# Performance work log

Measured on AMD Instinct MI355X. Metric: run time of the kernel, lower is better.

## Reference

```python
import jax, jax.numpy as jnp
import numpy as np

CS = [32, 32, 64, 128, 256, 256, 128, 96, 96]
NC = 19
N0, N1, N2, N3, N4 = 50000, 20000, 8000, 3200, 1300


def build_shapes():
    cs = CS
    def rb(ci, co):
        t = [(27, ci, co), (27, co, co)]
        if ci != co:
            t.append((ci, co))  # 1x1 shortcut conv
        return t
    s = [(27, 4, cs[0]), (27, cs[0], cs[0])]                       # stem
    s += [(8, cs[0], cs[0])] + rb(cs[0], cs[1]) + rb(cs[1], cs[1])  # stage1
    s += [(8, cs[1], cs[1])] + rb(cs[1], cs[2]) + rb(cs[2], cs[2])  # stage2
    s += [(8, cs[2], cs[2])] + rb(cs[2], cs[3]) + rb(cs[3], cs[3])  # stage3
    s += [(8, cs[3], cs[3])] + rb(cs[3], cs[4]) + rb(cs[4], cs[4])  # stage4
    s += [(8, cs[4], cs[5])] + rb(cs[5] + cs[3], cs[5]) + rb(cs[5], cs[5])  # up1
    s += [(8, cs[5], cs[6])] + rb(cs[6] + cs[2], cs[6]) + rb(cs[6], cs[6])  # up2
    s += [(8, cs[6], cs[7])] + rb(cs[7] + cs[1], cs[7]) + rb(cs[7], cs[7])  # up3
    s += [(8, cs[7], cs[8])] + rb(cs[8] + cs[0], cs[8]) + rb(cs[8], cs[8])  # up4
    s += [(cs[8], NC), (NC,), (cs[8], cs[8]), (cs[8],), (cs[8], 128), (128,)]
    return s

P_TOTAL = sum(int(np.prod(sh)) for sh in build_shapes())


def _bn(x):
    # train-mode BatchNorm, gamma=1 beta=0 (set by weight_initialization)
    return (x - x.mean(0)) * jax.lax.rsqrt(jnp.var(x, 0) + 1e-5)


def _spconv(x, nbr, W):
    # sparse conv as gather-GEMM-scatter over K kernel offsets.
    # x: [Nin, Cin], nbr: [Nout, K] row indices into x, W: [K, Cin, Cout]
    acc0 = jnp.zeros((nbr.shape[0], W.shape[-1]), x.dtype)
    def step(acc, kw):
        idx, Wk = kw
        return acc + x[idx] @ Wk, None
    acc, _ = jax.lax.scan(step, acc0, (nbr.T, W))
    return acc


def _spdeconv(x, parent, off, W):
    # transposed ks=2 stride=2 conv: each fine voxel has exactly one coarse
    # parent and one kernel-offset id. out[i] = x[parent[i]] @ W[off[i]]
    y = jnp.einsum('nc,kcd->nkd', x[parent], W)  # [Nf, 8, Cout]
    return jnp.take_along_axis(y, off[:, None, None], axis=1)[:, 0, :]


def _cbr(x, nbr, W):
    return jax.nn.relu(_bn(_spconv(x, nbr, W)))


def _resblock(x, nbr, take, ci, co):
    w1 = take(); w2 = take()
    h = _bn(_spconv(jax.nn.relu(_bn(_spconv(x, nbr, w1))), nbr, w2))
    s = x if ci == co else _bn(x @ take())
    return jax.nn.relu(h + s)


def _forward(x, nbr0, nbr1, nbr2, nbr3, nbr4, d1, d2, d3, d4,
             u1p, u1o, u2p, u2o, u3p, u3o, u4p, u4o, params):
    parts = []
    o = 0
    for sh in build_shapes():
        n = int(np.prod(sh))
        parts.append(params[o:o + n].reshape(sh))
        o += n
    it = iter(parts)
    take = lambda: next(it)
    cs = CS
    x0 = _cbr(x, nbr0, take()); x0 = _cbr(x0, nbr0, take())            # stem
    h = _cbr(x0, d1, take())
    h = _resblock(h, nbr1, take, cs[0], cs[1]); x1 = _resblock(h, nbr1, take, cs[1], cs[1])
    h = _cbr(x1, d2, take())
    h = _resblock(h, nbr2, take, cs[1], cs[2]); x2 = _resblock(h, nbr2, take, cs[2], cs[2])
    h = _cbr(x2, d3, take())
    h = _resblock(h, nbr3, take, cs[2], cs[3]); x3 = _resblock(h, nbr3, take, cs[3], cs[3])
    h = _cbr(x3, d4, take())
    h = _resblock(h, nbr4, take, cs[3], cs[4]); x4 = _resblock(h, nbr4, take, cs[4], cs[4])
    y = jax.nn.relu(_bn(_spdeconv(x4, u1p, u1o, take())))
    y = jnp.concatenate([y, x3], 1)
    y = _resblock(y, nbr3, take, cs[5] + cs[3], cs[5]); y = _resblock(y, nbr3, take, cs[5], cs[5])
    y = jax.nn.relu(_bn(_spdeconv(y, u2p, u2o, take())))
    y = jnp.concatenate([y, x2], 1)
    y = _resblock(y, nbr2, take, cs[6] + cs[2], cs[6]); y = _resblock(y, nbr2, take, cs[6], cs[6])
    y = jax.nn.relu(_bn(_spdeconv(y, u3p, u3o, take())))
    y = jnp.concatenate([y, x1], 1)
    y = _resblock(y, nbr1, take, cs[7] + cs[1], cs[7]); y = _resblock(y, nbr1, take, cs[7], cs[7])
    y = jax.nn.relu(_bn(_spdeconv(y, u4p, u4o, take())))
    y = jnp.concatenate([y, x0], 1)
    y = _resblock(y, nbr0, take, cs[8] + cs[0], cs[8]); y = _resblock(y, nbr0, take, cs[8], cs[8])
    wc = take(); bc = take(); w1 = take(); b1 = take(); w2 = take(); b2 = take()
    out = y @ wc + bc                             # classifier logits [N0, NC]
    feat = jax.nn.relu(y @ w1 + b1) @ w2 + b2     # projection head [N0, 128]
    return out, feat


def setup_inputs() -> dict:
    key = jax.random.key(0)
    ks = jax.random.split(key, 20)
    ri = lambda k, shape, hi: jax.random.randint(k, shape, 0, hi, dtype=jnp.int32)
    return {
        'x': jax.random.normal(ks[0], (N0, 4), jnp.float32),
        'nbr0': ri(ks[1], (N0, 27), N0), 'nbr1': ri(ks[2], (N1, 27), N1),
        'nbr2': ri(ks[3], (N2, 27), N2), 'nbr3': ri(ks[4], (N3, 27), N3),
        'nbr4': ri(ks[5], (N4, 27), N4),
        'd1': ri(ks[6], (N1, 8), N0), 'd2': ri(ks[7], (N2, 8), N1),
        'd3': ri(ks[8], (N3, 8), N2), 'd4': ri(ks[9], (N4, 8), N3),
        'u1p': ri(ks[10], (N3,), N4), 'u1o': ri(ks[11], (N3,), 8),
        'u2p': ri(ks[12], (N2,), N3), 'u2o': ri(ks[13], (N2,), 8),
        'u3p': ri(ks[14], (N1,), N2), 'u3o': ri(ks[15], (N1,), 8),
        'u4p': ri(ks[16], (N0,), N1), 'u4o': ri(ks[17], (N0,), 8),
        'params': jax.random.normal(ks[18], (P_TOTAL,), jnp.float32) * 0.05,
    }


def reference(x, nbr0, nbr1, nbr2, nbr3, nbr4, d1, d2, d3, d4,
              u1p, u1o, u2p, u2o, u3p, u3o, u4p, u4o, params):
    return _forward(x, nbr0, nbr1, nbr2, nbr3, nbr4, d1, d2, d3, d4,
                    u1p, u1o, u2p, u2o, u3p, u3o, u4p, u4o, params)
```

## Files before the change

kernel.cpp:

```cpp
#include <hip/hip_runtime.h>
#include <hip/hip_bf16.h>
#include <stdint.h>

typedef __hip_bfloat16 hbf;
typedef unsigned short u16;
typedef __attribute__((ext_vector_type(8))) short bfrag;
typedef __attribute__((ext_vector_type(4))) float f4;

#define NP0 50000
#define NP1 20000
#define NP2 8000
#define NP3 3200
#define NP4 1300

static inline int cdiv(int a, int b) { return (a + b - 1) / b; }

static __device__ __forceinline__ float u2f(u16 u) { return __uint_as_float(((unsigned)u) << 16); }
static __device__ __forceinline__ u16 f2u(float f) {
  hbf h = __float2bfloat16(f);
  u16 r; __builtin_memcpy(&r, &h, 2); return r;
}
static __device__ __forceinline__ float pload(const void* P, int isbf, size_t i) {
  return isbf ? u2f(((const u16*)P)[i]) : ((const float*)P)[i];
}


struct PrepD {
  long cpre;
  long src;
  long dst;
  int K, CI, CO, CB32, NT16, pad;
};

__global__ void k_sniff(const void* __restrict__ xraw, int* __restrict__ flagp) {
  __shared__ float smax[256];
  const u16* u = (const u16*)xraw;
  float m = 0.f;
  for (int i = threadIdx.x; i < 2048; i += 256) {
    float v = u2f(u[2 * i]);
    if (isnan(v) || isinf(v)) m = 1e30f; else m = fmaxf(m, fabsf(v));
  }
  smax[threadIdx.x] = m;
  __syncthreads();
  for (int s = 128; s > 0; s >>= 1) {
    if (threadIdx.x < s) smax[threadIdx.x] = fmaxf(smax[threadIdx.x], smax[threadIdx.x + s]);
    __syncthreads();
  }
  if (threadIdx.x == 0) *flagp = (smax[0] < 1e4f) ? 1 : 0;
}

__global__ __launch_bounds__(256) void k_prep_all(
    const void* __restrict__ P, const int* __restrict__ flagp, u16* __restrict__ W,
    const PrepD* __restrict__ T, int NL, long totalC, long totalE)
{
  int f = *flagp;
  int L = 0;
  for (long c = (long)blockIdx.x * 256 + threadIdx.x; c < totalC; c += (long)gridDim.x * 256) {
    while (L + 1 < NL && c >= T[L + 1].cpre) ++L;
    PrepD d = T[L];
    long lc = c - d.cpre;
    int lane = (int)(lc & 63); long t = lc >> 6;
    int nt = (int)(t % d.NT16); t /= d.NT16;
    int cb = (int)(t % d.CB32); int k = (int)(t / d.CB32);
    int co = nt * 16 + (lane & 15);
    int cib = cb * 32 + (lane >> 4) * 8;
    u16 hi[8], lo[8];
#pragma unroll
    for (int j = 0; j < 8; ++j) {
      int ci = cib + j; float v = 0.f;
      if (ci < d.CI && co < d.CO) v = pload(P, f, d.src + ((size_t)k * d.CI + ci) * d.CO + co);
      u16 h = f2u(v);
      hi[j] = h;
      lo[j] = f2u(v - u2f(h));
    }
    *(bfrag*)(W + d.dst + lc * 8) = *(const bfrag*)hi;
    *(bfrag*)(W + totalE + d.dst + lc * 8) = *(const bfrag*)lo;
  }
}

__global__ __launch_bounds__(256) void k_prep_frag(
    const void* __restrict__ P, const int* __restrict__ flagp, u16* __restrict__ W,
    long src, long halfel, int K, int CI, int CO, int CB32, int NT16)
{
  int f = *flagp;
  long total = (long)K * CB32 * NT16 * 64;
  for (long c = (long)blockIdx.x * 256 + threadIdx.x; c < total; c += (long)gridDim.x * 256) {
    int lane = (int)(c & 63); long t = c >> 6;
    int nt = (int)(t % NT16); t /= NT16;
    int cb = (int)(t % CB32); int k = (int)(t / CB32);
    int co = nt * 16 + (lane & 15);
    int cib = cb * 32 + (lane >> 4) * 8;
    u16 hi[8], lo[8];
#pragma unroll
    for (int j = 0; j < 8; ++j) {
      int ci = cib + j; float v = 0.f;
      if (ci < CI && co < CO) v = pload(P, f, src + ((size_t)k * CI + ci) * CO + co);
      u16 h = f2u(v);
      hi[j] = h;
      lo[j] = f2u(v - u2f(h));
    }
    *(bfrag*)(W + c * 8) = *(const bfrag*)hi;
    *(bfrag*)(W + halfel + c * 8) = *(const bfrag*)lo;
  }
}

__global__ void k_prep_bias(const void* __restrict__ P, const int* __restrict__ flagp,
                            float* __restrict__ B, long src, int n)
{
  int f = *flagp;
  int i = blockIdx.x * 256 + threadIdx.x;
  if (i < n) B[i] = pload(P, f, src + i);
}

__global__ void k_pad(const void* __restrict__ xraw, const int* __restrict__ flagp,
                      float* __restrict__ Xp, int N)
{
  int f = *flagp; int total = N * 32;
  for (int i = blockIdx.x * 256 + threadIdx.x; i < total; i += gridDim.x * 256) {
    int n = i >> 5, cc = i & 31;
    Xp[i] = (cc < 4) ? pload(xraw, f, (size_t)n * 4 + cc) : 0.f;
  }
}

template<int NT>
__global__ __launch_bounds__(256) void k_conv_mfma(
    const float* __restrict__ X, const int* __restrict__ nbr,
    const u16* __restrict__ Wp, long halfel, float* __restrict__ Y,
    const float* __restrict__ bias, int relu, const int* __restrict__ flagp,
    int N, int K, int CB32, int NT16, int CO, int XS, int tlen, int atomic)
{
  const int f = *flagp;
  const int lane = threadIdx.x & 63;
  const int wv = threadIdx.x >> 6;
  const int rowbase = blockIdx.x * 128 + wv * 32;
  const int ntb = blockIdx.y * NT;
  const int ml = lane & 15;
  const int quad = lane >> 4;
  const int ktot = K * CB32;
  const int t0 = blockIdx.z * tlen;
  const int t1 = (t0 + tlen < ktot) ? (t0 + tlen) : ktot;

  f4 acc[2][NT];
#pragma unroll
  for (int i = 0; i < 2; ++i)
#pragma unroll
    for (int j = 0; j < NT; ++j) acc[i][j] = (f4)(0.f);

  int k = t0 / CB32;
  int cb = t0 - k * CB32;
  int idx[2];
  bool fresh = true;

  if (f) {
    for (int t = t0; t < t1; ++t) {
      if (fresh) {
#pragma unroll
        for (int mt = 0; mt < 2; ++mt) {
          int r = rowbase + mt * 16 + ml;
          idx[mt] = (r < N) ? (nbr ? nbr[(size_t)r * K + k] : r) : 0;
        }
        fresh = false;
      }
      const u16* WH = Wp + (size_t)t * NT16 * 512;
      bfrag bh[NT];
#pragma unroll
      for (int nt = 0; nt < NT; ++nt) {
        size_t o = ((size_t)(ntb + nt) * 64 + lane) * 8;
        bh[nt] = *(const bfrag*)(WH + o);
      }
      bfrag ahi[2], alo[2];
#pragma unroll
      for (int mt = 0; mt < 2; ++mt) {
        const float* ap = X + (size_t)idx[mt] * XS + cb * 32 + quad * 8;
        float4 q0 = *(const float4*)ap;
        float4 q1 = *(const float4*)(ap + 4);
        float av[8] = {q0.x, q0.y, q0.z, q0.w, q1.x, q1.y, q1.z, q1.w};
        u16 hi8[8], lo8[8];
#pragma unroll
        for (int j = 0; j < 8; ++j) {
          u16 hh = f2u(av[j]);
          hi8[j] = hh;
          lo8[j] = f2u(av[j] - u2f(hh));
        }
        __builtin_memcpy(&ahi[mt], hi8, 16);
        __builtin_memcpy(&alo[mt], lo8, 16);
      }
#pragma unroll
      for (int mt = 0; mt < 2; ++mt)
#pragma unroll
        for (int nt = 0; nt < NT; ++nt) {
          acc[mt][nt] = __builtin_amdgcn_mfma_f32_16x16x32_bf16(alo[mt], bh[nt], acc[mt][nt], 0, 0, 0);
          acc[mt][nt] = __builtin_amdgcn_mfma_f32_16x16x32_bf16(ahi[mt], bh[nt], acc[mt][nt], 0, 0, 0);
        }
      if (++cb == CB32) { cb = 0; ++k; fresh = true; }
    }
  } else {
    for (int t = t0; t < t1; ++t) {
      if (fresh) {
#pragma unroll
        for (int mt = 0; mt < 2; ++mt) {
          int r = rowbase + mt * 16 + ml;
          idx[mt] = (r < N) ? (nbr ? nbr[(size_t)r * K + k] : r) : 0;
        }
        fresh = false;
      }
      const u16* WH = Wp + (size_t)t * NT16 * 512;
      const u16* WL = WH + halfel;
      bfrag bh[NT], bl[NT];
#pragma unroll
      for (int nt = 0; nt < NT; ++nt) {
        size_t o = ((size_t)(ntb + nt) * 64 + lane) * 8;
        bh[nt] = *(const bfrag*)(WH + o);
        bl[nt] = *(const bfrag*)(WL + o);
      }
      bfrag ahi[2], alo[2];
#pragma unroll
      for (int mt = 0; mt < 2; ++mt) {
        const float* ap = X + (size_t)idx[mt] * XS + cb * 32 + quad * 8;
        float4 q0 = *(const float4*)ap;
        float4 q1 = *(const float4*)(ap + 4);
        float av[8] = {q0.x, q0.y, q0.z, q0.w, q1.x, q1.y, q1.z, q1.w};
        u16 hi8[8], lo8[8];
#pragma unroll
        for (int j = 0; j < 8; ++j) {
          u16 hh = f2u(av[j]);
          hi8[j] = hh;
          lo8[j] = f2u(av[j] - u2f(hh));
        }
        __builtin_memcpy(&ahi[mt], hi8, 16);
        __builtin_memcpy(&alo[mt], lo8, 16);
      }
#pragma unroll
      for (int mt = 0; mt < 2; ++mt)
#pragma unroll
        for (int nt = 0; nt < NT; ++nt) {
          acc[mt][nt] = __builtin_amdgcn_mfma_f32_16x16x32_bf16(alo[mt], bh[nt], acc[mt][nt], 0, 0, 0);
          acc[mt][nt] = __builtin_amdgcn_mfma_f32_16x16x32_bf16(ahi[mt], bl[nt], acc[mt][nt], 0, 0, 0);
          acc[mt][nt] = __builtin_amdgcn_mfma_f32_16x16x32_bf16(ahi[mt], bh[nt], acc[mt][nt], 0, 0, 0);
        }
      if (++cb == CB32) { cb = 0; ++k; fresh = true; }
    }
  }

#pragma unroll
  for (int mt = 0; mt < 2; ++mt) {
#pragma unroll
    for (int nt = 0; nt < NT; ++nt) {
      int col = (ntb + nt) * 16 + ml;
      if (col >= CO) continue;
      float bvv = bias ? bias[col] : 0.f;
#pragma unroll
      for (int reg = 0; reg < 4; ++reg) {
        int row = rowbase + mt * 16 + quad * 4 + reg;
        if (row < N) {
          if (atomic) {
            atomicAdd(&Y[(size_t)row * CO + col], acc[mt][nt][reg]);
          } else {
            float v = acc[mt][nt][reg] + bvv;
            if (relu) v = fmaxf(v, 0.f);
            Y[(size_t)row * CO + col] = v;
          }
        }
      }
    }
  }
}

__global__ void k_bias_relu(float* __restrict__ Y, const float* __restrict__ bias,
                            int relu, int total, int CO)
{
  int stride = gridDim.x * 256;
  for (int i = blockIdx.x * 256 + threadIdx.x; i < total; i += stride) {
    int c = i % CO;
    float v = Y[i] + (bias ? bias[c] : 0.f);
    if (relu) v = fmaxf(v, 0.f);
    Y[i] = v;
  }
}

static void launch_conv(hipStream_t s, int bx, const float* X, const int* nbr,
                        const u16* W, long halfel, float* Y, const float* bias, int relu,
                        const int* flagp, int N, int K, int CB32, int NT16, int CO, int XS)
{
  int NT = (NT16 % 6 == 0) ? 6 : ((NT16 % 4 == 0) ? 4 : 2);
  int ny = NT16 / NT;
  int ktot = K * CB32;
  long blocks = (long)bx * ny;
  int ZS = 1;
  if (ktot > 1) {
    ZS = (int)((1024 + blocks - 1) / blocks);
    if (ZS > ktot) ZS = ktot;
    if (ZS < 1) ZS = 1;
  }
  int tlen = cdiv(ktot, ZS);
  ZS = cdiv(ktot, tlen);
  int atomic = (ZS > 1) ? 1 : 0;
  if (atomic) hipMemsetAsync(Y, 0, (size_t)N * CO * 4, s);
  dim3 g(bx, ny, ZS);
  if (NT == 6)      k_conv_mfma<6><<<g, 256, 0, s>>>(X, nbr, W, halfel, Y, bias, relu, flagp, N, K, CB32, NT16, CO, XS, tlen, atomic);
  else if (NT == 4) k_conv_mfma<4><<<g, 256, 0, s>>>(X, nbr, W, halfel, Y, bias, relu, flagp, N, K, CB32, NT16, CO, XS, tlen, atomic);
  else              k_conv_mfma<2><<<g, 256, 0, s>>>(X, nbr, W, halfel, Y, bias, relu, flagp, N, K, CB32, NT16, CO, XS, tlen, atomic);
  if (atomic && (bias || relu)) {
    int total = N * CO;
    int nb = cdiv(total, 1024); if (nb > 1024) nb = 1024; if (nb < 1) nb = 1;
    k_bias_relu<<<nb, 256, 0, s>>>(Y, bias, relu, total, CO);
  }
}

__global__ __launch_bounds__(256) void k_deconv(
    const float* __restrict__ X, const int* __restrict__ par, const int* __restrict__ off,
    const void* __restrict__ P, long wofs, const int* __restrict__ flagp,
    float* __restrict__ Y, int N, int CI, int CO)
{
  int f = *flagp;
  int lane = threadIdx.x & 63, wv = threadIdx.x >> 6;
  int n = blockIdx.y * 4 + wv; if (n >= N) return;
  int co = blockIdx.x * 64 + lane; if (co >= CO) return;
  const float* xr = X + (size_t)par[n] * CI;
  size_t wbase = wofs + (size_t)off[n] * CI * CO + co;
  float acc = 0.f;
  for (int ci = 0; ci < CI; ci += 4) {
    float4 xv = *(const float4*)(xr + ci);
    acc += xv.x * pload(P, f, wbase + (size_t)ci * CO);
    acc += xv.y * pload(P, f, wbase + (size_t)(ci + 1) * CO);
    acc += xv.z * pload(P, f, wbase + (size_t)(ci + 2) * CO);
    acc += xv.w * pload(P, f, wbase + (size_t)(ci + 3) * CO);
  }
  Y[(size_t)n * CO + co] = acc;
}

__global__ __launch_bounds__(256) void k_bn_stats(
    const float* __restrict__ X, float* __restrict__ st, int total, int C)
{
  __shared__ float ssum[384], ssq[384];
  for (int c = threadIdx.x; c < C; c += 256) { ssum[c] = 0.f; ssq[c] = 0.f; }
  __syncthreads();
  int gid = blockIdx.x * 256 + threadIdx.x;
  int total4 = total >> 2;
  int stride = gridDim.x * 256;
  int c0 = (gid * 4) % C;
  float s0 = 0.f, s1 = 0.f, s2 = 0.f, s3 = 0.f;
  float q0 = 0.f, q1 = 0.f, q2 = 0.f, q3 = 0.f;
  for (int i = gid; i < total4; i += stride) {
    float4 v = ((const float4*)X)[i];
    s0 += v.x; q0 += v.x * v.x;
    s1 += v.y; q1 += v.y * v.y;
    s2 += v.z; q2 += v.z * v.z;
    s3 += v.w; q3 += v.w * v.w;
  }
  atomicAdd(&ssum[c0], s0);     atomicAdd(&ssq[c0], q0);
  atomicAdd(&ssum[c0 + 1], s1); atomicAdd(&ssq[c0 + 1], q1);
  atomicAdd(&ssum[c0 + 2], s2); atomicAdd(&ssq[c0 + 2], q2);
  atomicAdd(&ssum[c0 + 3], s3); atomicAdd(&ssq[c0 + 3], q3);
  __syncthreads();
  for (int c = threadIdx.x; c < C; c += 256) {
    atomicAdd(&st[c], ssum[c]); atomicAdd(&st[384 + c], ssq[c]);
  }
}

__global__ __launch_bounds__(256) void k_bn_apply(
    const float* __restrict__ X, const float* __restrict__ st, const float* __restrict__ add,
    float* __restrict__ Y, int relu, int total, int C, float invN)
{
  __shared__ float mean[384], rsig[384];
  for (int c = threadIdx.x; c < C; c += 256) {
    float mm = st[c] * invN;
    float vv = st[384 + c] * invN - mm * mm;
    mean[c] = mm; rsig[c] = rsqrtf(vv + 1e-5f);
  }
  __syncthreads();
  int gid = blockIdx.x * 256 + threadIdx.x;
  int total4 = total >> 2;
  int stride = gridDim.x * 256;
  int c0 = (gid * 4) % C;
  float m0 = mean[c0], m1 = mean[c0 + 1], m2 = mean[c0 + 2], m3 = mean[c0 + 3];
  float r0 = rsig[c0], r1 = rsig[c0 + 1], r2 = rsig[c0 + 2], r3 = rsig[c0 + 3];
  for (int i = gid; i < total4; i += stride) {
    float4 v = ((const float4*)X)[i];
    v.x = (v.x - m0) * r0; v.y = (v.y - m1) * r1;
    v.z = (v.z - m2) * r2; v.w = (v.w - m3) * r3;
    if (add) {
      float4 a = ((const float4*)add)[i];
      v.x += a.x; v.y += a.y; v.z += a.z; v.w += a.w;
    }
    if (relu) {
      v.x = fmaxf(v.x, 0.f); v.y = fmaxf(v.y, 0.f);
      v.z = fmaxf(v.z, 0.f); v.w = fmaxf(v.w, 0.f);
    }
    ((float4*)Y)[i] = v;
  }
}

__global__ void k_copycols(const float* __restrict__ S, float* __restrict__ D,
                           int N, int Cs, int Cd, int off)
{
  int csq = Cs >> 2;
  int total4 = N * csq;
  int stride = gridDim.x * 256;
  for (int i = blockIdx.x * 256 + threadIdx.x; i < total4; i += stride) {
    int n = i / csq, cc = i - n * csq;
    ((float4*)D)[((size_t)n * Cd + off) / 4 + cc] = ((const float4*)S)[i];
  }
}

__global__ void k_store_dyn(const float* __restrict__ S, void* __restrict__ D,
                            const int* __restrict__ flagp, size_t eofs, int n)
{
  int f = *flagp;
  int n4 = n >> 2;
  int stride = gridDim.x * 256;
  for (int i = blockIdx.x * 256 + threadIdx.x; i < n4; i += stride) {
    float4 v = ((const float4*)S)[i];
    if (f) {
      ushort4 u;
      u.x = f2u(v.x); u.y = f2u(v.y); u.z = f2u(v.z); u.w = f2u(v.w);
      *(ushort4*)((u16*)D + eofs + (size_t)i * 4) = u;
    } else {
      *(float4*)((float*)D + eofs + (size_t)i * 4) = v;
    }
  }
}

static int build_table(PrepD* T, long* totalC, long* totalE) {
  int n = 0; long po = 0, ce = 0, cc = 0;
  auto W = [&](int K, int CI, int CO) {
    int CB = cdiv(CI, 32), NTx = cdiv(CO, 16);
    long ch = (long)K * CB * NTx * 64;
    T[n].cpre = cc; T[n].src = po; T[n].dst = ce;
    T[n].K = K; T[n].CI = CI; T[n].CO = CO; T[n].CB32 = CB; T[n].NT16 = NTx; T[n].pad = 0;
    ++n; cc += ch; ce += ch * 8; po += (long)K * CI * CO;
  };
  auto SKIP = [&](long e) { po += e; };
  W(27, 4, 32); W(27, 32, 32);
  W(8, 32, 32); W(27, 32, 32); W(27, 32, 32); W(27, 32, 32); W(27, 32, 32);
  W(8, 32, 32); W(27, 32, 64); W(27, 64, 64); W(1, 32, 64); W(27, 64, 64); W(27, 64, 64);
  W(8, 64, 64); W(27, 64, 128); W(27, 128, 128); W(1, 64, 128); W(27, 128, 128); W(27, 128, 128);
  W(8, 128, 128); W(27, 128, 256); W(27, 256, 256); W(1, 128, 256); W(27, 256, 256); W(27, 256, 256);
  SKIP(8L * 256 * 256);
  W(27, 384, 256); W(27, 256, 256); W(1, 384, 256); W(27, 256, 256); W(27, 256, 256);
  SKIP(8L * 256 * 128);
  W(27, 192, 128); W(27, 128, 128); W(1, 192, 128); W(27, 128, 128); W(27, 128, 128);
  SKIP(8L * 128 * 96);
  W(27, 128, 96); W(27, 96, 96); W(1, 128, 96); W(27, 96, 96); W(27, 96, 96);
  SKIP(8L * 96 * 96);
  W(27, 128, 96); W(27, 96, 96); W(1, 128, 96); W(27, 96, 96); W(27, 96, 96);
  W(1, 96, 19); SKIP(19); W(1, 96, 96); SKIP(96); W(1, 96, 128); SKIP(128);
  *totalC = cc; *totalE = ce;
  return n;
}


extern "C" void kernel_launch(void* const* d_in, const int* in_sizes, int n_in,
                              void* d_out, int out_size, void* d_ws, size_t ws_size,
                              hipStream_t stream)
{
  const void* xraw = d_in[0];
  const int* nbr0 = (const int*)d_in[1];
  const int* nbr1 = (const int*)d_in[2];
  const int* nbr2 = (const int*)d_in[3];
  const int* nbr3 = (const int*)d_in[4];
  const int* nbr4 = (const int*)d_in[5];
  const int* d1 = (const int*)d_in[6];
  const int* d2 = (const int*)d_in[7];
  const int* d3 = (const int*)d_in[8];
  const int* d4 = (const int*)d_in[9];
  const int* u1p = (const int*)d_in[10]; const int* u1o = (const int*)d_in[11];
  const int* u2p = (const int*)d_in[12]; const int* u2o = (const int*)d_in[13];
  const int* u3p = (const int*)d_in[14]; const int* u3o = (const int*)d_in[15];
  const int* u4p = (const int*)d_in[16]; const int* u4o = (const int*)d_in[17];
  const void* params = d_in[18];
  (void)in_sizes; (void)n_in;

  static PrepD h_table[64];
  long totalC = 0, totalE = 0;
  int NL = build_table(h_table, &totalC, &totalE);

  char* base = (char*)d_ws; size_t off = 0;
  auto ab = [&](size_t bytes) -> void* { void* p = base + off; off += (bytes + 63) & ~(size_t)63; return p; };
  int* flagp = (int*)ab(64);
  float* st = (float*)ab((size_t)64 * 768 * 4);
  float* Bstf = (float*)ab((size_t)512 * 4);
  float* x0 = (float*)ab((size_t)NP0 * 32 * 4);
  float* x1 = (float*)ab((size_t)NP1 * 32 * 4);
  float* x2 = (float*)ab((size_t)NP2 * 64 * 4);
  float* x3 = (float*)ab((size_t)NP3 * 128 * 4);
  float* x4 = (float*)ab((size_t)NP4 * 256 * 4);
  float* U  = (float*)ab((size_t)NP0 * 96 * 4);
  float* A  = (float*)ab((size_t)NP0 * 96 * 4);
  float* B  = (float*)ab((size_t)NP0 * 128 * 4);
  float* Xp = B;

  size_t wall_bytes = (size_t)totalE * 4;
  size_t rem = (ws_size > off) ? (ws_size - off) : 0;
  bool bigprep = rem >= wall_bytes + 8192;
  u16* Wall = nullptr; PrepD* d_table = nullptr; u16* Wst = nullptr;
  if (bigprep) {
    Wall = (u16*)ab(wall_bytes);
    d_table = (PrepD*)ab(4096);
  } else {
    Wst = (u16*)ab((size_t)5400000 * 2);
  }
  if (off > ws_size) { hipMemsetAsync(d_out, 0, (size_t)out_size * 2, stream); return; }

  long po = 0;
  int bnc = 0;
  int wli = 0;

  auto prepF = [&](int K, int CI, int CO, int CB32, int NT16) -> long {
    long chunks = (long)K * CB32 * NT16 * 64;
    long halfel = chunks * 8;
    int nb = (int)((chunks + 255) / 256); if (nb > 4096) nb = 4096; if (nb < 1) nb = 1;
    k_prep_frag<<<nb, 256, 0, stream>>>(params, flagp, Wst, po, halfel, K, CI, CO, CB32, NT16);
    po += (long)K * CI * CO;
    return halfel;
  };
  auto getW = [&](int K, int CI, int CO, int CB32, int NT16, const u16** Wp, long* he) {
    if (bigprep) {
      *Wp = Wall + h_table[wli].dst; *he = totalE;
      ++wli; po += (long)K * CI * CO;
    } else {
      *he = prepF(K, CI, CO, CB32, NT16); *Wp = Wst;
    }
  };
  auto convop = [&](const float* X, const int* nb_, int K, int CI, int CO, float* Y, int N, int XS) {
    int CB32 = cdiv(CI, 32), NT16 = cdiv(CO, 16);
    const u16* Wp; long he;
    getW(K, CI, CO, CB32, NT16, &Wp, &he);
    launch_conv(stream, cdiv(N, 128), X, nb_, Wp, he, Y, nullptr, 0, flagp, N, K, CB32, NT16, CO, XS);
  };
  auto linop = [&](const float* X, int CI, int CO, float* Y, int N, bool bias, int relu) {
    int CB32 = cdiv(CI, 32), NT16 = cdiv(CO, 16);
    const u16* Wp; long he;
    getW(1, CI, CO, CB32, NT16, &Wp, &he);
    const float* bp = nullptr;
    if (bias) {
      k_prep_bias<<<cdiv(CO, 256), 256, 0, stream>>>(params, flagp, Bstf, po, CO);
      po += CO; bp = Bstf;
    }
    launch_conv(stream, cdiv(N, 128), X, nullptr, Wp, he, Y, bp, relu, flagp, N, 1, CB32, NT16, CO, CI);
  };
  auto deconvop = [&](const float* X, const int* par, const int* ofv, int CI, int CO, float* Y, int N) {
    long wofs = po; po += (long)8 * CI * CO;
    dim3 g(cdiv(CO, 64), cdiv(N, 4));
    k_deconv<<<g, 256, 0, stream>>>(X, par, ofv, params, wofs, flagp, Y, N, CI, CO);
  };
  auto bnop = [&](const float* X, int N, int C, const float* add, int relu, float* out) {
    float* slot = st + (size_t)(bnc++) * 768;
    int total = N * C;
    int total4 = total >> 2;
    int nb1 = cdiv(total4, 4096); if (nb1 > 504) nb1 = 504; if (nb1 < 3) nb1 = 3;
    nb1 = ((nb1 + 2) / 3) * 3;
    k_bn_stats<<<nb1, 256, 0, stream>>>(X, slot, total, C);
    int nb2 = cdiv(total4, 2048); if (nb2 > 510) nb2 = 510; if (nb2 < 3) nb2 = 3;
    nb2 = ((nb2 + 2) / 3) * 3;
    k_bn_apply<<<nb2, 256, 0, stream>>>(X, slot, add, out ? out : (float*)X, relu, total, C, 1.0f / (float)N);
  };
  auto copyop = [&](const float* S, float* D, int N, int Cs, int Cd, int o2) {
    int total4 = (N * Cs) >> 2;
    int nb3 = cdiv(total4, 1024); if (nb3 > 1024) nb3 = 1024; if (nb3 < 1) nb3 = 1;
    k_copycols<<<nb3, 256, 0, stream>>>(S, D, N, Cs, Cd, o2);
  };
  auto storeop = [&](const float* S, size_t eo, int n) {
    int nb4 = cdiv(n >> 2, 1024); if (nb4 > 1024) nb4 = 1024; if (nb4 < 1) nb4 = 1;
    k_store_dyn<<<nb4, 256, 0, stream>>>(S, d_out, flagp, eo, n);
  };
  auto resblock = [&](const int* nb, int N, int CI, int CO,
                      float* H, float* t1, float* t2, float* OUT) {
    convop(H, nb, 27, CI, CO, t1, N, CI);
    bnop(t1, N, CO, nullptr, 1, nullptr);
    convop(t1, nb, 27, CO, CO, t2, N, CO);
    const float* S;
    if (CI == CO) S = H;
    else { linop(H, CI, CO, t1, N, false, 0); bnop(t1, N, CO, nullptr, 0, nullptr); S = t1; }
    bnop(t2, N, CO, S, 1, OUT);
  };

  k_sniff<<<1, 256, 0, stream>>>(xraw, flagp);
  if (bigprep) {
    hipMemcpyAsync(d_table, h_table, (size_t)NL * sizeof(PrepD), hipMemcpyHostToDevice, stream);
    int nbp = (int)((totalC + 255) / 256); if (nbp > 4096) nbp = 4096;
    k_prep_all<<<nbp, 256, 0, stream>>>(params, flagp, Wall, d_table, NL, totalC, totalE);
  }
  hipMemsetAsync(st, 0, (size_t)64 * 768 * 4, stream);
  k_pad<<<1024, 256, 0, stream>>>(xraw, flagp, Xp, NP0);

  convop(Xp, nbr0, 27, 4, 32, A, NP0, 32);  bnop(A, NP0, 32, nullptr, 1, nullptr);
  convop(A, nbr0, 27, 32, 32, x0, NP0, 32); bnop(x0, NP0, 32, nullptr, 1, nullptr);
  convop(x0, d1, 8, 32, 32, U, NP1, 32); bnop(U, NP1, 32, nullptr, 1, nullptr);
  resblock(nbr1, NP1, 32, 32, U, A, B, U);
  resblock(nbr1, NP1, 32, 32, U, A, B, x1);
  convop(x1, d2, 8, 32, 32, U, NP2, 32); bnop(U, NP2, 32, nullptr, 1, nullptr);
  resblock(nbr2, NP2, 32, 64, U, A, B, U);
  resblock(nbr2, NP2, 64, 64, U, A, B, x2);
  convop(x2, d3, 8, 64, 64, U, NP3, 64); bnop(U, NP3, 64, nullptr, 1, nullptr);
  resblock(nbr3, NP3, 64, 128, U, A, B, U);
  resblock(nbr3, NP3, 128, 128, U, A, B, x3);
  convop(x3, d4, 8, 128, 128, U, NP4, 128); bnop(U, NP4, 128, nullptr, 1, nullptr);
  resblock(nbr4, NP4, 128, 256, U, A, B, U);
  resblock(nbr4, NP4, 256, 256, U, A, B, x4);
  deconvop(x4, u1p, u1o, 256, 256, A, NP3); bnop(A, NP3, 256, nullptr, 1, nullptr);
  copyop(A, B, NP3, 256, 384, 0); copyop(x3, B, NP3, 128, 384, 256);
  resblock(nbr3, NP3, 384, 256, B, A, U, B);
  resblock(nbr3, NP3, 256, 256, B, A, U, U);
  deconvop(U, u2p, u2o, 256, 128, A, NP2); bnop(A, NP2, 128, nullptr, 1, nullptr);
  copyop(A, B, NP2, 128, 192, 0); copyop(x2, B, NP2, 64, 192, 128);
  resblock(nbr2, NP2, 192, 128, B, A, U, B);
  resblock(nbr2, NP2, 128, 128, B, A, U, U);
  deconvop(U, u3p, u3o, 128, 96, A, NP1); bnop(A, NP1, 96, nullptr, 1, nullptr);
  copyop(A, B, NP1, 96, 128, 0); copyop(x1, B, NP1, 32, 128, 96);
  resblock(nbr1, NP1, 128, 96, B, A, U, B);
  resblock(nbr1, NP1, 96, 96, B, A, U, U);
  deconvop(U, u4p, u4o, 96, 96, A, NP0); bnop(A, NP0, 96, nullptr, 1, nullptr);
  copyop(A, B, NP0, 96, 128, 0); copyop(x0, B, NP0, 32, 128, 96);
  resblock(nbr0, NP0, 128, 96, B, A, U, B);
  resblock(nbr0, NP0, 96, 96, B, A, U, U);
  linop(U, 96, 19, x0, NP0, true, 0);
  linop(U, 96, 96, A, NP0, true, 1);
  linop(A, 96, 128, B, NP0, true, 0);
  storeop(x0, 0, NP0 * 19);
  storeop(B, (size_t)NP0 * 19, NP0 * 128);
}
```

Baseline: 4.298 ms.

## Store activations in fp16 and run convs as fp16 MFMA with split weights

Intermediate activations are now stored as fp16 instead of fp32. Conv kernels load fp16 fragments directly and issue f16 MFMAs, which drops the per-element hi/lo bf16 split of activations and cuts the MFMA count per tile. Weights are packed as fp16 hi/lo pairs. The transposed convs now build an 8-wide gather index table that points at a zero row and reuse the MFMA conv path, replacing the scalar deconv kernel. BN apply, residual adds and column concatenation work on fp16 buffers, halving activation traffic in exchange for fp16 range and precision limits on activations.

```diff
diff --git a/kernel.cpp b/kernel.cpp
--- a/kernel.cpp
+++ b/kernel.cpp
@@ -5,6 +5,7 @@
 typedef __hip_bfloat16 hbf;
 typedef unsigned short u16;
 typedef __attribute__((ext_vector_type(8))) short bfrag;
+typedef _Float16 __attribute__((ext_vector_type(8))) hfrag;
 typedef __attribute__((ext_vector_type(4))) float f4;
 
 #define NP0 50000
@@ -20,16 +21,21 @@
   hbf h = __float2bfloat16(f);
   u16 r; __builtin_memcpy(&r, &h, 2); return r;
 }
+static __device__ __forceinline__ u16 f2h(float f) {
+  _Float16 h = (_Float16)f;
+  u16 r; __builtin_memcpy(&r, &h, 2); return r;
+}
+static __device__ __forceinline__ float h2f(u16 u) {
+  _Float16 h; __builtin_memcpy(&h, &u, 2); return (float)h;
+}
 static __device__ __forceinline__ float pload(const void* P, int isbf, size_t i) {
   return isbf ? u2f(((const u16*)P)[i]) : ((const float*)P)[i];
 }
 
 
 struct PrepD {
-  long cpre;
-  long src;
-  long dst;
-  int K, CI, CO, CB32, NT16, pad;
+  long cpre, src, dst;
+  int K, CI, CO, CB32, NT16, hf;
 };
 
 __global__ void k_sniff(const void* __restrict__ xraw, int* __restrict__ flagp) {
@@ -69,9 +75,8 @@
     for (int j = 0; j < 8; ++j) {
       int ci = cib + j; float v = 0.f;
       if (ci < d.CI && co < d.CO) v = pload(P, f, d.src + ((size_t)k * d.CI + ci) * d.CO + co);
-      u16 h = f2u(v);
-      hi[j] = h;
-      lo[j] = f2u(v - u2f(h));
+      if (d.hf) { u16 h = f2h(v); hi[j] = h; lo[j] = f2h(v - h2f(h)); }
+      else      { u16 h = f2u(v); hi[j] = h; lo[j] = f2u(v - u2f(h)); }
     }
     *(bfrag*)(W + d.dst + lc * 8) = *(const bfrag*)hi;
     *(bfrag*)(W + totalE + d.dst + lc * 8) = *(const bfrag*)lo;
@@ -80,7 +85,7 @@
 
 __global__ __launch_bounds__(256) void k_prep_frag(
     const void* __restrict__ P, const int* __restrict__ flagp, u16* __restrict__ W,
-    long src, long halfel, int K, int CI, int CO, int CB32, int NT16)
+    long src, long halfel, int hf, int K, int CI, int CO, int CB32, int NT16)
 {
   int f = *flagp;
   long total = (long)K * CB32 * NT16 * 64;
@@ -95,9 +100,8 @@
     for (int j = 0; j < 8; ++j) {
       int ci = cib + j; float v = 0.f;
       if (ci < CI && co < CO) v = pload(P, f, src + ((size_t)k * CI + ci) * CO + co);
-      u16 h = f2u(v);
-      hi[j] = h;
-      lo[j] = f2u(v - u2f(h));
+      if (hf) { u16 h = f2h(v); hi[j] = h; lo[j] = f2h(v - h2f(h)); }
+      else    { u16 h = f2u(v); hi[j] = h; lo[j] = f2u(v - u2f(h)); }
     }
     *(bfrag*)(W + c * 8) = *(const bfrag*)hi;
     *(bfrag*)(W + halfel + c * 8) = *(const bfrag*)lo;
@@ -113,18 +117,30 @@
 }
 
 __global__ void k_pad(const void* __restrict__ xraw, const int* __restrict__ flagp,
-                      float* __restrict__ Xp, int N)
+                      u16* __restrict__ Xp, int N)
 {
   int f = *flagp; int total = N * 32;
   for (int i = blockIdx.x * 256 + threadIdx.x; i < total; i += gridDim.x * 256) {
     int n = i >> 5, cc = i & 31;
-    Xp[i] = (cc < 4) ? pload(xraw, f, (size_t)n * 4 + cc) : 0.f;
+    float v = (cc < 4) ? pload(xraw, f, (size_t)n * 4 + cc) : 0.f;
+    Xp[i] = f2h(v);
+  }
+}
+
+__global__ void k_mk_didx(const int* __restrict__ par, const int* __restrict__ off,
+                          int* __restrict__ idx, int N, int ZR)
+{
+  int stride = gridDim.x * 256;
+  for (int i = blockIdx.x * 256 + threadIdx.x; i < N; i += stride) {
+    int p = par[i], o = off[i];
+#pragma unroll
+    for (int k = 0; k < 8; ++k) idx[(size_t)i * 8 + k] = (k == o) ? p : ZR;
   }
 }
 
 template<int NT>
 __global__ __launch_bounds__(256) void k_conv_mfma(
-    const float* __restrict__ X, const int* __restrict__ nbr,
+    const void* __restrict__ Xv, const int* __restrict__ nbr,
     const u16* __restrict__ Wp, long halfel, float* __restrict__ Y,
     const float* __restrict__ bias, int relu, const int* __restrict__ flagp,
     int N, int K, int CB32, int NT16, int CO, int XS, int tlen, int atomic)
@@ -139,6 +155,7 @@
   const int ktot = K * CB32;
   const int t0 = blockIdx.z * tlen;
   const int t1 = (t0 + tlen < ktot) ? (t0 + tlen) : ktot;
+  if (t0 >= t1) return;
 
   f4 acc[2][NT];
 #pragma unroll
@@ -150,6 +167,7 @@
   int cb = t0 - k * CB32;
   int idx[2];
   bool fresh = true;
+  const u16* X = (const u16*)Xv;
 
   if (f) {
     for (int t = t0; t < t1; ++t) {
@@ -162,36 +180,19 @@
         fresh = false;
       }
       const u16* WH = Wp + (size_t)t * NT16 * 512;
-      bfrag bh[NT];
-#pragma unroll
-      for (int nt = 0; nt < NT; ++nt) {
-        size_t o = ((size_t)(ntb + nt) * 64 + lane) * 8;
-        bh[nt] = *(const bfrag*)(WH + o);
-      }
-      bfrag ahi[2], alo[2];
-#pragma unroll
-      for (int mt = 0; mt < 2; ++mt) {
-        const float* ap = X + (size_t)idx[mt] * XS + cb * 32 + quad * 8;
-        float4 q0 = *(const float4*)ap;
-        float4 q1 = *(const float4*)(ap + 4);
-        float av[8] = {q0.x, q0.y, q0.z, q0.w, q1.x, q1.y, q1.z, q1.w};
-        u16 hi8[8], lo8[8];
-#pragma unroll
-        for (int j = 0; j < 8; ++j) {
-          u16 hh = f2u(av[j]);
-          hi8[j] = hh;
-          lo8[j] = f2u(av[j] - u2f(hh));
-        }
-        __builtin_memcpy(&ahi[mt], hi8, 16);
-        __builtin_memcpy(&alo[mt], lo8, 16);
-      }
+      hfrag bh[NT];
+#pragma unroll
+      for (int nt = 0; nt < NT; ++nt)
+        bh[nt] = *(const hfrag*)(WH + ((size_t)(ntb + nt) * 64 + lane) * 8);
+      hfrag a[2];
 #pragma unroll
       for (int mt = 0; mt < 2; ++mt)
-#pragma unroll
-        for (int nt = 0; nt < NT; ++nt) {
-          acc[mt][nt] = __builtin_amdgcn_mfma_f32_16x16x32_bf16(alo[mt], bh[nt], acc[mt][nt], 0, 0, 0);
-          acc[mt][nt] = __builtin_amdgcn_mfma_f32_16x16x32_bf16(ahi[mt], bh[nt], acc[mt][nt], 0, 0, 0);
-        }
+        a[mt] = *(const hfrag*)(X + (size_t)idx[mt] * XS + cb * 32 + quad * 8);
+#pragma unroll
+      for (int mt = 0; mt < 2; ++mt)
+#pragma unroll
+        for (int nt = 0; nt < NT; ++nt)
+          acc[mt][nt] = __builtin_amdgcn_mfma_f32_16x16x32_f16(a[mt], bh[nt], acc[mt][nt], 0, 0, 0);
       if (++cb == CB32) { cb = 0; ++k; fresh = true; }
     }
   } else {
@@ -206,37 +207,23 @@
       }
       const u16* WH = Wp + (size_t)t * NT16 * 512;
       const u16* WL = WH + halfel;
-      bfrag bh[NT], bl[NT];
+      hfrag bh[NT], bl[NT];
 #pragma unroll
       for (int nt = 0; nt < NT; ++nt) {
         size_t o = ((size_t)(ntb + nt) * 64 + lane) * 8;
-        bh[nt] = *(const bfrag*)(WH + o);
-        bl[nt] = *(const bfrag*)(WL + o);
+        bh[nt] = *(const hfrag*)(WH + o);
+        bl[nt] = *(const hfrag*)(WL + o);
       }
-      bfrag ahi[2], alo[2];
-#pragma unroll
-      for (int mt = 0; mt < 2; ++mt) {
-        const float* ap = X + (size_t)idx[mt] * XS + cb * 32 + quad * 8;
-        float4 q0 = *(const float4*)ap;
-        float4 q1 = *(const float4*)(ap + 4);
-        float av[8] = {q0.x, q0.y, q0.z, q0.w, q1.x, q1.y, q1.z, q1.w};
-        u16 hi8[8], lo8[8];
-#pragma unroll
-        for (int j = 0; j < 8; ++j) {
-          u16 hh = f2u(av[j]);
-          hi8[j] = hh;
-          lo8[j] = f2u(av[j] - u2f(hh));
-        }
-        __builtin_memcpy(&ahi[mt], hi8, 16);
-        __builtin_memcpy(&alo[mt], lo8, 16);
-      }
+      hfrag a[2];
 #pragma unroll
       for (int mt = 0; mt < 2; ++mt)
+        a[mt] = *(const hfrag*)(X + (size_t)idx[mt] * XS + cb * 32 + quad * 8);
+#pragma unroll
+      for (int mt = 0; mt < 2; ++mt)
 #pragma unroll
         for (int nt = 0; nt < NT; ++nt) {
-          acc[mt][nt] = __builtin_amdgcn_mfma_f32_16x16x32_bf16(alo[mt], bh[nt], acc[mt][nt], 0, 0, 0);
-          acc[mt][nt] = __builtin_amdgcn_mfma_f32_16x16x32_bf16(ahi[mt], bl[nt], acc[mt][nt], 0, 0, 0);
-          acc[mt][nt] = __builtin_amdgcn_mfma_f32_16x16x32_bf16(ahi[mt], bh[nt], acc[mt][nt], 0, 0, 0);
+          acc[mt][nt] = __builtin_amdgcn_mfma_f32_16x16x32_f16(a[mt], bl[nt], acc[mt][nt], 0, 0, 0);
+          acc[mt][nt] = __builtin_amdgcn_mfma_f32_16x16x32_f16(a[mt], bh[nt], acc[mt][nt], 0, 0, 0);
         }
       if (++cb == CB32) { cb = 0; ++k; fresh = true; }
     }
@@ -267,7 +254,7 @@
 }
 
 __global__ void k_bias_relu(float* __restrict__ Y, const float* __restrict__ bias,
-                            int relu, int total, int CO)
+                            u16* __restrict__ d16, int relu, int total, int CO)
 {
   int stride = gridDim.x * 256;
   for (int i = blockIdx.x * 256 + threadIdx.x; i < total; i += stride) {
@@ -275,12 +262,14 @@
     float v = Y[i] + (bias ? bias[c] : 0.f);
     if (relu) v = fmaxf(v, 0.f);
     Y[i] = v;
-  }
-}
-
-static void launch_conv(hipStream_t s, int bx, const float* X, const int* nbr,
+    if (d16) d16[i] = f2h(v);
+  }
+}
+
+static void launch_conv(hipStream_t s, int bx, const void* X, const int* nbr,
                         const u16* W, long halfel, float* Y, const float* bias, int relu,
-                        const int* flagp, int N, int K, int CB32, int NT16, int CO, int XS)
+                        const int* flagp, int N, int K, int CB32, int NT16, int CO, int XS,
+                        u16* d16)
 {
   int NT = (NT16 % 6 == 0) ? 6 : ((NT16 % 4 == 0) ? 4 : 2);
   int ny = NT16 / NT;
@@ -300,33 +289,11 @@
   if (NT == 6)      k_conv_mfma<6><<<g, 256, 0, s>>>(X, nbr, W, halfel, Y, bias, relu, flagp, N, K, CB32, NT16, CO, XS, tlen, atomic);
   else if (NT == 4) k_conv_mfma<4><<<g, 256, 0, s>>>(X, nbr, W, halfel, Y, bias, relu, flagp, N, K, CB32, NT16, CO, XS, tlen, atomic);
   else              k_conv_mfma<2><<<g, 256, 0, s>>>(X, nbr, W, halfel, Y, bias, relu, flagp, N, K, CB32, NT16, CO, XS, tlen, atomic);
-  if (atomic && (bias || relu)) {
+  if ((atomic && (bias || relu)) || d16) {
     int total = N * CO;
     int nb = cdiv(total, 1024); if (nb > 1024) nb = 1024; if (nb < 1) nb = 1;
-    k_bias_relu<<<nb, 256, 0, s>>>(Y, bias, relu, total, CO);
-  }
-}
-
-__global__ __launch_bounds__(256) void k_deconv(
-    const float* __restrict__ X, const int* __restrict__ par, const int* __restrict__ off,
-    const void* __restrict__ P, long wofs, const int* __restrict__ flagp,
-    float* __restrict__ Y, int N, int CI, int CO)
-{
-  int f = *flagp;
-  int lane = threadIdx.x & 63, wv = threadIdx.x >> 6;
-  int n = blockIdx.y * 4 + wv; if (n >= N) return;
-  int co = blockIdx.x * 64 + lane; if (co >= CO) return;
-  const float* xr = X + (size_t)par[n] * CI;
-  size_t wbase = wofs + (size_t)off[n] * CI * CO + co;
-  float acc = 0.f;
-  for (int ci = 0; ci < CI; ci += 4) {
-    float4 xv = *(const float4*)(xr + ci);
-    acc += xv.x * pload(P, f, wbase + (size_t)ci * CO);
-    acc += xv.y * pload(P, f, wbase + (size_t)(ci + 1) * CO);
-    acc += xv.z * pload(P, f, wbase + (size_t)(ci + 2) * CO);
-    acc += xv.w * pload(P, f, wbase + (size_t)(ci + 3) * CO);
-  }
-  Y[(size_t)n * CO + co] = acc;
+    k_bias_relu<<<nb, 256, 0, s>>>(Y, atomic ? bias : nullptr, d16, atomic ? relu : 0, total, CO);
+  }
 }
 
 __global__ __launch_bounds__(256) void k_bn_stats(
@@ -359,8 +326,9 @@
 }
 
 __global__ __launch_bounds__(256) void k_bn_apply(
-    const float* __restrict__ X, const float* __restrict__ st, const float* __restrict__ add,
-    float* __restrict__ Y, int relu, int total, int C, float invN)
+    const float* __restrict__ X, const float* __restrict__ st,
+    const u16* __restrict__ add2, u16* __restrict__ Y2,
+    int relu, int total, int C, float invN)
 {
   __shared__ float mean[384], rsig[384];
   for (int c = threadIdx.x; c < C; c += 256) {
@@ -377,29 +345,30 @@
   float r0 = rsig[c0], r1 = rsig[c0 + 1], r2 = rsig[c0 + 2], r3 = rsig[c0 + 3];
   for (int i = gid; i < total4; i += stride) {
     float4 v = ((const float4*)X)[i];
-    v.x = (v.x - m0) * r0; v.y = (v.y - m1) * r1;
-    v.z = (v.z - m2) * r2; v.w = (v.w - m3) * r3;
-    if (add) {
-      float4 a = ((const float4*)add)[i];
-      v.x += a.x; v.y += a.y; v.z += a.z; v.w += a.w;
+    float w0 = (v.x - m0) * r0, w1 = (v.y - m1) * r1;
+    float w2 = (v.z - m2) * r2, w3 = (v.w - m3) * r3;
+    if (add2) {
+      ushort4 ah = *(const ushort4*)(add2 + (size_t)i * 4);
+      w0 += h2f(ah.x); w1 += h2f(ah.y); w2 += h2f(ah.z); w3 += h2f(ah.w);
     }
     if (relu) {
-      v.x = fmaxf(v.x, 0.f); v.y = fmaxf(v.y, 0.f);
-      v.z = fmaxf(v.z, 0.f); v.w = fmaxf(v.w, 0.f);
-    }
-    ((float4*)Y)[i] = v;
-  }
-}
-
-__global__ void k_copycols(const float* __restrict__ S, float* __restrict__ D,
+      w0 = fmaxf(w0, 0.f); w1 = fmaxf(w1, 0.f);
+      w2 = fmaxf(w2, 0.f); w3 = fmaxf(w3, 0.f);
+    }
+    ushort4 hh; hh.x = f2h(w0); hh.y = f2h(w1); hh.z = f2h(w2); hh.w = f2h(w3);
+    *(ushort4*)(Y2 + (size_t)i * 4) = hh;
+  }
+}
+
+__global__ void k_copycols(const u16* __restrict__ S, u16* __restrict__ D,
                            int N, int Cs, int Cd, int off)
 {
   int csq = Cs >> 2;
   int total4 = N * csq;
   int stride = gridDim.x * 256;
   for (int i = blockIdx.x * 256 + threadIdx.x; i < total4; i += stride) {
-    int n = i / csq, cc = i - n * csq;
-    ((float4*)D)[((size_t)n * Cd + off) / 4 + cc] = ((const float4*)S)[i];
+    int n = i / csq, cc = (i - n * csq) * 4;
+    *(ushort4*)(D + (size_t)n * Cd + off + cc) = *(const ushort4*)(S + (size_t)i * 4);
   }
 }
 
@@ -427,7 +396,7 @@
     int CB = cdiv(CI, 32), NTx = cdiv(CO, 16);
     long ch = (long)K * CB * NTx * 64;
     T[n].cpre = cc; T[n].src = po; T[n].dst = ce;
-    T[n].K = K; T[n].CI = CI; T[n].CO = CO; T[n].CB32 = CB; T[n].NT16 = NTx; T[n].pad = 0;
+    T[n].K = K; T[n].CI = CI; T[n].CO = CO; T[n].CB32 = CB; T[n].NT16 = NTx; T[n].hf = 1;
     ++n; cc += ch; ce += ch * 8; po += (long)K * CI * CO;
   };
   auto SKIP = [&](long e) { po += e; };
@@ -436,19 +405,18 @@
   W(8, 32, 32); W(27, 32, 64); W(27, 64, 64); W(1, 32, 64); W(27, 64, 64); W(27, 64, 64);
   W(8, 64, 64); W(27, 64, 128); W(27, 128, 128); W(1, 64, 128); W(27, 128, 128); W(27, 128, 128);
   W(8, 128, 128); W(27, 128, 256); W(27, 256, 256); W(1, 128, 256); W(27, 256, 256); W(27, 256, 256);
-  SKIP(8L * 256 * 256);
+  W(8, 256, 256);
   W(27, 384, 256); W(27, 256, 256); W(1, 384, 256); W(27, 256, 256); W(27, 256, 256);
-  SKIP(8L * 256 * 128);
+  W(8, 256, 128);
   W(27, 192, 128); W(27, 128, 128); W(1, 192, 128); W(27, 128, 128); W(27, 128, 128);
-  SKIP(8L * 128 * 96);
+  W(8, 128, 96);
   W(27, 128, 96); W(27, 96, 96); W(1, 128, 96); W(27, 96, 96); W(27, 96, 96);
-  SKIP(8L * 96 * 96);
+  W(8, 96, 96);
   W(27, 128, 96); W(27, 96, 96); W(1, 128, 96); W(27, 96, 96); W(27, 96, 96);
   W(1, 96, 19); SKIP(19); W(1, 96, 96); SKIP(96); W(1, 96, 128); SKIP(128);
   *totalC = cc; *totalE = ce;
   return n;
 }
-
 
 extern "C" void kernel_launch(void* const* d_in, const int* in_sizes, int n_in,
                               void* d_out, int out_size, void* d_ws, size_t ws_size,
@@ -480,15 +448,16 @@
   int* flagp = (int*)ab(64);
   float* st = (float*)ab((size_t)64 * 768 * 4);
   float* Bstf = (float*)ab((size_t)512 * 4);
-  float* x0 = (float*)ab((size_t)NP0 * 32 * 4);
-  float* x1 = (float*)ab((size_t)NP1 * 32 * 4);
-  float* x2 = (float*)ab((size_t)NP2 * 64 * 4);
-  float* x3 = (float*)ab((size_t)NP3 * 128 * 4);
-  float* x4 = (float*)ab((size_t)NP4 * 256 * 4);
-  float* U  = (float*)ab((size_t)NP0 * 96 * 4);
+  int* didx = (int*)ab((size_t)NP0 * 8 * 4);
+  u16* x0 = (u16*)ab((size_t)(NP0 + 1) * 32 * 2);
+  u16* x1 = (u16*)ab((size_t)NP1 * 32 * 2);
+  u16* x2 = (u16*)ab((size_t)NP2 * 64 * 2);
+  u16* x3 = (u16*)ab((size_t)NP3 * 128 * 2);
+  u16* x4 = (u16*)ab((size_t)(NP4 + 1) * 256 * 2);
+  float* U  = (float*)ab((size_t)(NP0 + 1) * 96 * 4);
   float* A  = (float*)ab((size_t)NP0 * 96 * 4);
   float* B  = (float*)ab((size_t)NP0 * 128 * 4);
-  float* Xp = B;
+  u16* Xp = (u16*)B;
 
   size_t wall_bytes = (size_t)totalE * 4;
   size_t rem = (ws_size > off) ? (ws_size - off) : 0;
@@ -510,7 +479,7 @@
     long chunks = (long)K * CB32 * NT16 * 64;
     long halfel = chunks * 8;
     int nb = (int)((chunks + 255) / 256); if (nb > 4096) nb = 4096; if (nb < 1) nb = 1;
-    k_prep_frag<<<nb, 256, 0, stream>>>(params, flagp, Wst, po, halfel, K, CI, CO, CB32, NT16);
+    k_prep_frag<<<nb, 256, 0, stream>>>(params, flagp, Wst, po, halfel, 1, K, CI, CO, CB32, NT16);
     po += (long)K * CI * CO;
     return halfel;
   };
@@ -522,13 +491,13 @@
       *he = prepF(K, CI, CO, CB32, NT16); *Wp = Wst;
     }
   };
-  auto convop = [&](const float* X, const int* nb_, int K, int CI, int CO, float* Y, int N, int XS) {
+  auto convop = [&](const u16* X, const int* nb_, int K, int CI, int CO, float* Y, int N, int XS) {
     int CB32 = cdiv(CI, 32), NT16 = cdiv(CO, 16);
     const u16* Wp; long he;
     getW(K, CI, CO, CB32, NT16, &Wp, &he);
-    launch_conv(stream, cdiv(N, 128), X, nb_, Wp, he, Y, nullptr, 0, flagp, N, K, CB32, NT16, CO, XS);
-  };
-  auto linop = [&](const float* X, int CI, int CO, float* Y, int N, bool bias, int relu) {
+    launch_conv(stream, cdiv(N, 128), X, nb_, Wp, he, Y, nullptr, 0, flagp, N, K, CB32, NT16, CO, XS, nullptr);
+  };
+  auto linop = [&](const u16* X, int CI, int CO, float* Y, int N, bool bias, int relu, u16* d16) {
     int CB32 = cdiv(CI, 32), NT16 = cdiv(CO, 16);
     const u16* Wp; long he;
     getW(1, CI, CO, CB32, NT16, &Wp, &he);
@@ -537,14 +506,16 @@
       k_prep_bias<<<cdiv(CO, 256), 256, 0, stream>>>(params, flagp, Bstf, po, CO);
       po += CO; bp = Bstf;
     }
-    launch_conv(stream, cdiv(N, 128), X, nullptr, Wp, he, Y, bp, relu, flagp, N, 1, CB32, NT16, CO, CI);
-  };
-  auto deconvop = [&](const float* X, const int* par, const int* ofv, int CI, int CO, float* Y, int N) {
-    long wofs = po; po += (long)8 * CI * CO;
-    dim3 g(cdiv(CO, 64), cdiv(N, 4));
-    k_deconv<<<g, 256, 0, stream>>>(X, par, ofv, params, wofs, flagp, Y, N, CI, CO);
-  };
-  auto bnop = [&](const float* X, int N, int C, const float* add, int relu, float* out) {
+    launch_conv(stream, cdiv(N, 128), X, nullptr, Wp, he, Y, bp, relu, flagp, N, 1, CB32, NT16, CO, CI, d16);
+  };
+  auto deconvop = [&](const u16* X, int Ns, const int* par, const int* ofv,
+                      int CI, int CO, float* Y, int N) {
+    hipMemsetAsync((void*)(X + (size_t)Ns * CI), 0, (size_t)CI * 2, stream);
+    int nbl = cdiv(N, 256); if (nbl > 1024) nbl = 1024; if (nbl < 1) nbl = 1;
+    k_mk_didx<<<nbl, 256, 0, stream>>>(par, ofv, didx, N, Ns);
+    convop(X, didx, 8, CI, CO, Y, N, CI);
+  };
+  auto bnop = [&](const float* X, int N, int C, const u16* add2, int relu, u16* out2) {
     float* slot = st + (size_t)(bnc++) * 768;
     int total = N * C;
     int total4 = total >> 2;
@@ -553,9 +524,9 @@
     k_bn_stats<<<nb1, 256, 0, stream>>>(X, slot, total, C);
     int nb2 = cdiv(total4, 2048); if (nb2 > 510) nb2 = 510; if (nb2 < 3) nb2 = 3;
     nb2 = ((nb2 + 2) / 3) * 3;
-    k_bn_apply<<<nb2, 256, 0, stream>>>(X, slot, add, out ? out : (float*)X, relu, total, C, 1.0f / (float)N);
-  };
-  auto copyop = [&](const float* S, float* D, int N, int Cs, int Cd, int o2) {
+    k_bn_apply<<<nb2, 256, 0, stream>>>(X, slot, add2, out2, relu, total, C, 1.0f / (float)N);
+  };
+  auto copyop = [&](const u16* S, u16* D, int N, int Cs, int Cd, int o2) {
     int total4 = (N * Cs) >> 2;
     int nb3 = cdiv(total4, 1024); if (nb3 > 1024) nb3 = 1024; if (nb3 < 1) nb3 = 1;
     k_copycols<<<nb3, 256, 0, stream>>>(S, D, N, Cs, Cd, o2);
@@ -564,15 +535,18 @@
     int nb4 = cdiv(n >> 2, 1024); if (nb4 > 1024) nb4 = 1024; if (nb4 < 1) nb4 = 1;
     k_store_dyn<<<nb4, 256, 0, stream>>>(S, d_out, flagp, eo, n);
   };
-  auto resblock = [&](const int* nb, int N, int CI, int CO,
-                      float* H, float* t1, float* t2, float* OUT) {
-    convop(H, nb, 27, CI, CO, t1, N, CI);
-    bnop(t1, N, CO, nullptr, 1, nullptr);
-    convop(t1, nb, 27, CO, CO, t2, N, CO);
-    const float* S;
-    if (CI == CO) S = H;
-    else { linop(H, CI, CO, t1, N, false, 0); bnop(t1, N, CO, nullptr, 0, nullptr); S = t1; }
-    bnop(t2, N, CO, S, 1, OUT);
+  auto resblock16 = [&](const int* nb, int N, int CI, int CO,
+                        u16* H16, float* t1, float* t2, u16* OUT16) {
+    convop(H16, nb, 27, CI, CO, t1, N, CI);
+    bnop(t1, N, CO, nullptr, 1, (u16*)t2);
+    convop((u16*)t2, nb, 27, CO, CO, t1, N, CO);
+    if (CI == CO) {
+      bnop(t1, N, CO, H16, 1, OUT16);
+    } else {
+      linop(H16, CI, CO, t2, N, false, 0, nullptr);
+      bnop(t2, N, CO, nullptr, 0, OUT16);
+      bnop(t1, N, CO, OUT16, 1, OUT16);
+    }
   };
 
   k_sniff<<<1, 256, 0, stream>>>(xraw, flagp);
@@ -584,39 +558,48 @@
   hipMemsetAsync(st, 0, (size_t)64 * 768 * 4, stream);
   k_pad<<<1024, 256, 0, stream>>>(xraw, flagp, Xp, NP0);
 
-  convop(Xp, nbr0, 27, 4, 32, A, NP0, 32);  bnop(A, NP0, 32, nullptr, 1, nullptr);
-  convop(A, nbr0, 27, 32, 32, x0, NP0, 32); bnop(x0, NP0, 32, nullptr, 1, nullptr);
-  convop(x0, d1, 8, 32, 32, U, NP1, 32); bnop(U, NP1, 32, nullptr, 1, nullptr);
-  resblock(nbr1, NP1, 32, 32, U, A, B, U);
-  resblock(nbr1, NP1, 32, 32, U, A, B, x1);
-  convop(x1, d2, 8, 32, 32, U, NP2, 32); bnop(U, NP2, 32, nullptr, 1, nullptr);
-  resblock(nbr2, NP2, 32, 64, U, A, B, U);
-  resblock(nbr2, NP2, 64, 64, U, A, B, x2);
-  convop(x2, d3, 8, 64, 64, U, NP3, 64); bnop(U, NP3, 64, nullptr, 1, nullptr);
-  resblock(nbr3, NP3, 64, 128, U, A, B, U);
-  resblock(nbr3, NP3, 128, 128, U, A, B, x3);
-  convop(x3, d4, 8, 128, 128, U, NP4, 128); bnop(U, NP4, 128, nullptr, 1, nullptr);
-  resblock(nbr4, NP4, 128, 256, U, A, B, U);
-  resblock(nbr4, NP4, 256, 256, U, A, B, x4);
-  deconvop(x4, u1p, u1o, 256, 256, A, NP3); bnop(A, NP3, 256, nullptr, 1, nullptr);
-  copyop(A, B, NP3, 256, 384, 0); copyop(x3, B, NP3, 128, 384, 256);
-  resblock(nbr3, NP3, 384, 256, B, A, U, B);
-  resblock(nbr3, NP3, 256, 256, B, A, U, U);
-  deconvop(U, u2p, u2o, 256, 128, A, NP2); bnop(A, NP2, 128, nullptr, 1, nullptr);
-  copyop(A, B, NP2, 128, 192, 0); copyop(x2, B, NP2, 64, 192, 128);
-  resblock(nbr2, NP2, 192, 128, B, A, U, B);
-  resblock(nbr2, NP2, 128, 128, B, A, U, U);
-  deconvop(U, u3p, u3o, 128, 96, A, NP1); bnop(A, NP1, 96, nullptr, 1, nullptr);
-  copyop(A, B, NP1, 96, 128, 0); copyop(x1, B, NP1, 32, 128, 96);
-  resblock(nbr1, NP1, 128, 96, B, A, U, B);
-  resblock(nbr1, NP1, 96, 96, B, A, U, U);
-  deconvop(U, u4p, u4o, 96, 96, A, NP0); bnop(A, NP0, 96, nullptr, 1, nullptr);
-  copyop(A, B, NP0, 96, 128, 0); copyop(x0, B, NP0, 32, 128, 96);
-  resblock(nbr0, NP0, 128, 96, B, A, U, B);
-  resblock(nbr0, NP0, 96, 96, B, A, U, U);
-  linop(U, 96, 19, x0, NP0, true, 0);
-  linop(U, 96, 96, A, NP0, true, 1);
-  linop(A, 96, 128, B, NP0, true, 0);
-  storeop(x0, 0, NP0 * 19);
+  u16* U16 = (u16*)U; u16* B16 = (u16*)B; u16* A16 = (u16*)A;
+
+  convop(Xp, nbr0, 27, 4, 32, A, NP0, 32);
+  bnop(A, NP0, 32, nullptr, 1, U16);
+  convop(U16, nbr0, 27, 32, 32, A, NP0, 32);
+  bnop(A, NP0, 32, nullptr, 1, x0);
+  convop(x0, d1, 8, 32, 32, A, NP1, 32); bnop(A, NP1, 32, nullptr, 1, U16);
+  resblock16(nbr1, NP1, 32, 32, U16, A, B, U16);
+  resblock16(nbr1, NP1, 32, 32, U16, A, B, x1);
+  convop(x1, d2, 8, 32, 32, A, NP2, 32); bnop(A, NP2, 32, nullptr, 1, U16);
+  resblock16(nbr2, NP2, 32, 64, U16, A, B, U16);
+  resblock16(nbr2, NP2, 64, 64, U16, A, B, x2);
+  convop(x2, d3, 8, 64, 64, A, NP3, 64); bnop(A, NP3, 64, nullptr, 1, U16);
+  resblock16(nbr3, NP3, 64, 128, U16, A, B, U16);
+  resblock16(nbr3, NP3, 128, 128, U16, A, B, x3);
+  convop(x3, d4, 8, 128, 128, A, NP4, 128); bnop(A, NP4, 128, nullptr, 1, U16);
+  resblock16(nbr4, NP4, 128, 256, U16, A, B, U16);
+  resblock16(nbr4, NP4, 256, 256, U16, A, B, x4);
+  deconvop(x4, NP4, u1p, u1o, 256, 256, A, NP3);
+  bnop(A, NP3, 256, nullptr, 1, U16);
+  copyop(U16, B16, NP3, 256, 384, 0); copyop(x3, B16, NP3, 128, 384, 256);
+  resblock16(nbr3, NP3, 384, 256, B16, A, U, B16);
+  resblock16(nbr3, NP3, 256, 256, B16, A, U, U16);
+  deconvop(U16, NP3, u2p, u2o, 256, 128, A, NP2);
+  bnop(A, NP2, 128, nullptr, 1, U16);
+  copyop(U16, B16, NP2, 128, 192, 0); copyop(x2, B16, NP2, 64, 192, 128);
+  resblock16(nbr2, NP2, 192, 128, B16, A, U, B16);
+  resblock16(nbr2, NP2, 128, 128, B16, A, U, U16);
+  deconvop(U16, NP2, u3p, u3o, 128, 96, A, NP1);
+  bnop(A, NP1, 96, nullptr, 1, U16);
+  copyop(U16, B16, NP1, 96, 128, 0); copyop(x1, B16, NP1, 32, 128, 96);
+  resblock16(nbr1, NP1, 128, 96, B16, A, U, B16);
+  resblock16(nbr1, NP1, 96, 96, B16, A, U, U16);
+  deconvop(U16, NP1, u4p, u4o, 96, 96, A, NP0);
+  bnop(A, NP0, 96, nullptr, 1, U16);
+  copyop(U16, B16, NP0, 96, 128, 0); copyop(x0, B16, NP0, 32, 128, 96);
+  resblock16(nbr0, NP0, 128, 96, B16, A, U, B16);
+  resblock16(nbr0, NP0, 96, 96, B16, A, U, U16);
+  float* x0f = (float*)x0;
+  linop(U16, 96, 19, x0f, NP0, true, 0, nullptr);
+  linop(U16, 96, 96, B, NP0, true, 1, A16);
+  linop(A16, 96, 128, B, NP0, true, 0, nullptr);
+  storeop(x0f, 0, NP0 * 19);
   storeop(B, (size_t)NP0 * 19, NP0 * 128);
 }
```

Result: faster. 3.701 ms (-13.9%).
